# Optimization experiments

Hardware: AMD Instinct MI355X
Metric: run time of the kernel (lower is better)

## Reference

```python
import jax, jax.numpy as jnp
import numpy as np

B, N, E_PER = 512, 256, 8192          # graphs, nodes per graph, edges per graph
FIN, H, K, FOUT = 128, 32, 16, 10     # in_channels, hidden, num clusters, out_channels
EPS = 1e-15


def setup_inputs() -> dict:
    key = jax.random.key(0)
    ks = jax.random.split(key, 12)
    x = jax.random.normal(ks[0], (B * N, FIN), jnp.float32)
    # intra-graph random edges, then offset into the global node index space
    src = jax.random.randint(ks[1], (B, E_PER), 0, N)
    dst = jax.random.randint(ks[2], (B, E_PER), 0, N)
    offs = (jnp.arange(B) * N)[:, None]
    edge_index = jnp.stack([(src + offs).reshape(-1), (dst + offs).reshape(-1)]).astype(jnp.int64)
    batch = jnp.repeat(jnp.arange(B), N).astype(jnp.int64)

    def lin(k, fin, fout):
        return (jax.random.normal(k, (fin, fout), jnp.float32) / np.sqrt(fin)).astype(jnp.float32)

    params = {
        'W_lin1': lin(ks[3], FIN, H), 'b_lin1': jnp.zeros((H,), jnp.float32),
        'W_rel1': lin(ks[4], H, H), 'b_rel1': jnp.zeros((H,), jnp.float32),
        'W_root1': lin(ks[5], H, H),
        'W_pool': lin(ks[6], H, K), 'b_pool': jnp.zeros((K,), jnp.float32),
        'W_rel2': lin(ks[7], H, H), 'b_rel2': jnp.zeros((H,), jnp.float32),
        'W_root2': lin(ks[8], H, H),
        'W_lin2': lin(ks[9], H, H), 'b_lin2': jnp.zeros((H,), jnp.float32),
        'W_lin3': lin(ks[10], H, FOUT), 'b_lin3': jnp.zeros((FOUT,), jnp.float32),
    }
    return {'x': x, 'edge_index': edge_index, 'batch': batch, **params}


def _densify(x, edge_index, batch):
    """to_dense_adj + to_dense_batch: [total,F] -> [B,N,F], [B,N,N], [B,N]."""
    n_total = x.shape[0]
    counts = jax.ops.segment_sum(jnp.ones((n_total,), jnp.int32), batch, num_segments=B)
    offsets = jnp.concatenate([jnp.zeros((1,), jnp.int32), jnp.cumsum(counts)[:-1]])
    pos = jnp.arange(n_total) - offsets[batch]            # position of node inside its graph
    eb = batch[edge_index[0]]                             # graph id of each edge
    adj = jnp.zeros((B, N, N), jnp.float32).at[eb, pos[edge_index[0]], pos[edge_index[1]]].add(1.0)
    xd = jnp.zeros((B, N, x.shape[1]), jnp.float32).at[batch, pos].set(x)
    mask = jnp.zeros((B, N), jnp.float32).at[batch, pos].set(1.0)
    return xd, adj, mask


def _dense_graph_conv(x, adj, W_rel, b_rel, W_root):
    # PyG DenseGraphConv(aggr='add'): lin_rel(adj @ x) + lin_root(x)
    return jnp.einsum('bnm,bmh,hk->bnk', adj, x, W_rel) + b_rel + x @ W_root


def _dense_mincut_pool(x, adj, s, mask):
    s = jax.nn.softmax(s, axis=-1)
    x = x * mask[..., None]
    s = s * mask[..., None]
    out = jnp.einsum('bnk,bnh->bkh', s, x)                        # s^T x
    out_adj = jnp.einsum('bnk,bnm,bmj->bkj', s, adj, s)           # s^T A s
    mincut_num = jnp.einsum('bkk->b', out_adj)
    d_flat = adj.sum(-1)                                          # degree
    mincut_den = jnp.einsum('bnk,bn,bnk->b', s, d_flat, s)        # trace(s^T D s)
    mincut_loss = jnp.mean(-(mincut_num / mincut_den))
    ss = jnp.einsum('bnk,bnj->bkj', s, s)
    ss_norm = jnp.linalg.norm(ss, axis=(-1, -2), keepdims=True)
    i_s = jnp.eye(K, dtype=jnp.float32)
    ortho_loss = jnp.mean(jnp.linalg.norm(ss / ss_norm - i_s / jnp.sqrt(jnp.float32(K)), axis=(-1, -2)))
    # zero diagonal, symmetric degree normalization
    diag_mask = 1.0 - i_s
    out_adj = out_adj * diag_mask
    d = jnp.sqrt(out_adj.sum(-1))[:, None, :] + EPS               # [B,1,K]
    out_adj = out_adj / d / jnp.swapaxes(d, 1, 2)
    return out, out_adj, mincut_loss, ortho_loss


def reference(x, edge_index, batch, W_lin1, b_lin1, W_rel1, b_rel1, W_root1,
              W_pool, b_pool, W_rel2, b_rel2, W_root2, W_lin2, b_lin2, W_lin3, b_lin3):
    xd, adj, mask = _densify(x, edge_index, batch)
    h = xd @ W_lin1 + b_lin1                                      # lin1
    h = _dense_graph_conv(h, adj, W_rel1, b_rel1, W_root1)        # conv1
    s2 = h @ W_pool + b_pool                                      # pool2
    h, adj_p, mincut_loss2, ortho_loss2 = _dense_mincut_pool(h, adj, s2, mask)
    h = _dense_graph_conv(h, adj_p, W_rel2, b_rel2, W_root2)      # conv2
    h = h.sum(axis=1)                                             # readout sum over clusters
    h = jax.nn.relu(h @ W_lin2 + b_lin2)
    h = h @ W_lin3 + b_lin3
    return jax.nn.log_softmax(h, axis=-1), mincut_loss2, ortho_loss2
```

## Files before the change

### kernel.cpp

```cpp
#include <hip/hip_runtime.h>

#define NB 512
#define NN 256
#define EPG 8192
#define FINC 128

typedef float f32x4 __attribute__((ext_vector_type(4)));
typedef short s16x8 __attribute__((ext_vector_type(8)));

__device__ __forceinline__ float bf2f(unsigned short u) {
  union { unsigned int i; float f; } x; x.i = ((unsigned int)u) << 16; return x.f;
}
__device__ __forceinline__ unsigned short f2bf(float f) {
  union { float f; unsigned int i; } x; x.f = f;
  unsigned int r = x.i + 0x7fffu + ((x.i >> 16) & 1u);
  return (unsigned short)(r >> 16);
}
__device__ __forceinline__ short ftrunc_bf(float f) {
  union { float f; unsigned int i; } x; x.f = f;
  return (short)(x.i >> 16);
}

struct Params {
  const void* x; const void* ei;
  const void *wl1, *bl1, *wr1, *br1, *wro1, *wp, *bp;
  const void *wr2, *br2, *wro2, *wl2, *bl2, *wl3, *bl3;
  float* out; float* ws;
};

__device__ __forceinline__ bool detect_bf16(const void* p) {
  const unsigned short* pw = (const unsigned short*)p;
  int sane = 0;
  for (int i = 0; i < 64; ++i) {
    unsigned e = (pw[i] >> 7) & 0xFFu;
    sane += (e > 96u && e < 132u) ? 1 : 0;
  }
  return sane >= 56;
}
__device__ __forceinline__ bool detect_i64(const void* p) {
  const int* pi = (const int*)p + EPG;
  int ok = 0;
  for (int i = 0; i < 32; ++i) ok += (pi[i] >= 256 && pi[i] < 512) ? 1 : 0;
  return ok < 24;
}
__device__ __forceinline__ float ldf(const void* p, int i, bool bf) {
  return bf ? bf2f(((const unsigned short*)p)[i]) : ((const float*)p)[i];
}

#define SMEM_TOTAL 81920

__global__ __launch_bounds__(1024, 8) void mincut_main(Params P) {
  extern __shared__ char smem[];
  const int t = threadIdx.x;
  const int b = blockIdx.x;

  const bool BF  = detect_bf16(P.wr1);
  const bool I64 = detect_i64(P.ei);

  float* pbufH  = (float*)(smem + 0);
  float* pbufL  = (float*)(smem + 2048);
  float* oadjH  = (float*)(smem + 4096);
  float* oadjL  = (float*)(smem + 5120);
  float* ssA    = (float*)(smem + 6144);
  float* pbuf   = (float*)(smem + 7168);
  float* oadjb  = (float*)(smem + 9216);
  unsigned short* h0T  = (unsigned short*)(smem + 33792);
  unsigned short* yTl  = (unsigned short*)(smem + 33792);
  unsigned short* h1Th = (unsigned short*)(smem + 33792);
  unsigned short* w1t  = (unsigned short*)(smem + 50688);
  unsigned short* zT   = (unsigned short*)(smem + 50688);
  unsigned short* sTh  = (unsigned short*)(smem + 50688);
  unsigned short* sTl  = (unsigned short*)(smem + 59136);
  unsigned short* wrelTh = (unsigned short*)(smem + 67584);
  unsigned short* wrelTl = (unsigned short*)(smem + 70144);
  unsigned short* wrootT = (unsigned short*)(smem + 72704);
  float* blin1f = (float*)(smem + 75264);
  unsigned short* yTh = (unsigned short*)(smem + 67584);
  unsigned short* taT = (unsigned short*)(smem + 67584);
  unsigned short* wpoolTh = (unsigned short*)(smem + 76032);
  unsigned short* wpoolTl = (unsigned short*)(smem + 77184);
  unsigned short* m1Th    = (unsigned short*)(smem + 78336);
  unsigned short* m1Tl    = (unsigned short*)(smem + 79488);
  float*          scrE    = (float*)(smem + 79488);
  unsigned short* m2Th    = (unsigned short*)(smem + 80640);
  float*          bMf     = (float*)(smem + 81792);
  unsigned short* brel1h  = (unsigned short*)(smem + 81856);

  const int wv = t >> 6, lane = t & 63;
  const int lm = lane & 15, quad = lane >> 4;
  const int mbase = wv * 16;

  {
    uint4 z = {0u, 0u, 0u, 0u};
    for (int i = t; i < 2112; i += 1024) ((uint4*)smem)[i] = z;
  }
  for (int e = t; e < 4096; e += 1024) {
    int k = e >> 5, c = e & 31;
    w1t[c * 136 + k] = f2bf(ldf(P.wl1, e, BF));
  }
  {
    int k = t >> 5, c = t & 31;
    float wr = ldf(P.wr1, t, BF);
    unsigned short hi = f2bf(wr);
    wrelTh[c * 40 + k] = hi;
    wrelTl[c * 40 + k] = f2bf(wr - bf2f(hi));
    wrootT[c * 40 + k] = f2bf(ldf(P.wro1, t, BF));
  }
  if (t < 512) {
    int m = t >> 4, c = t & 15;
    float w = ldf(P.wp, t, BF);
    unsigned short hi = f2bf(w);
    wpoolTh[c * 36 + m] = hi;
    wpoolTl[c * 36 + m] = f2bf(w - bf2f(hi));
  }
  if (t < 32) { blin1f[t] = ldf(P.bl1, t, BF); brel1h[t] = f2bf(ldf(P.br1, t, BF)); }
  __syncthreads();

  if (I64) {
    const uint4* s4 = (const uint4*)((const long long*)P.ei + (size_t)b * EPG) + t * 4;
    const uint4* d4 = (const uint4*)((const long long*)P.ei + (size_t)NB * EPG + (size_t)b * EPG) + t * 4;
    #pragma unroll
    for (int i = 0; i < 4; ++i) {
      uint4 a = s4[i], c = d4[i];
      unsigned n0 = (a.x & 255u) * 264u + (c.x & 255u);
      unsigned n1 = (a.z & 255u) * 264u + (c.z & 255u);
      atomicAdd((unsigned int*)(smem + ((n0 >> 3) << 2)), 1u << ((n0 & 7u) * 4u));
      atomicAdd((unsigned int*)(smem + ((n1 >> 3) << 2)), 1u << ((n1 & 7u) * 4u));
    }
  } else {
    const uint4* s4 = (const uint4*)((const int*)P.ei + (size_t)b * EPG) + t * 2;
    const uint4* d4 = (const uint4*)((const int*)P.ei + (size_t)NB * EPG + (size_t)b * EPG) + t * 2;
    #pragma unroll
    for (int i = 0; i < 2; ++i) {
      uint4 a = s4[i], c = d4[i];
      unsigned n0 = (a.x & 255u) * 264u + (c.x & 255u);
      unsigned n1 = (a.y & 255u) * 264u + (c.y & 255u);
      unsigned n2 = (a.z & 255u) * 264u + (c.z & 255u);
      unsigned n3 = (a.w & 255u) * 264u + (c.w & 255u);
      atomicAdd((unsigned int*)(smem + ((n0 >> 3) << 2)), 1u << ((n0 & 7u) * 4u));
      atomicAdd((unsigned int*)(smem + ((n1 >> 3) << 2)), 1u << ((n1 & 7u) * 4u));
      atomicAdd((unsigned int*)(smem + ((n2 >> 3) << 2)), 1u << ((n2 & 7u) * 4u));
      atomicAdd((unsigned int*)(smem + ((n3 >> 3) << 2)), 1u << ((n3 & 7u) * 4u));
    }
  }

  {
    f32x4 acc[2] = {{0.f,0.f,0.f,0.f},{0.f,0.f,0.f,0.f}};
    const size_t node = (size_t)(b * 256 + mbase + lm);
    #pragma unroll
    for (int ks = 0; ks < 4; ++ks) {
      const int k0 = ks * 32 + quad * 8;
      s16x8 a;
      if (BF) {
        a = *(const s16x8*)((const unsigned short*)P.x + node * 128 + k0);
      } else {
        const float* xp = (const float*)P.x + node * 128 + k0;
        f32x4 v0 = *(const f32x4*)xp;
        f32x4 v1 = *(const f32x4*)(xp + 4);
        #pragma unroll
        for (int j = 0; j < 4; ++j) { a[j] = (short)f2bf(v0[j]); a[4 + j] = (short)f2bf(v1[j]); }
      }
      #pragma unroll
      for (int ct = 0; ct < 2; ++ct) {
        s16x8 bh = *(const s16x8*)(w1t + (ct * 16 + lm) * 136 + k0);
        acc[ct] = __builtin_amdgcn_mfma_f32_16x16x32_bf16(a, bh, acc[ct], 0, 0, 0);
      }
    }
    #pragma unroll
    for (int ct = 0; ct < 2; ++ct) {
      const int c = ct * 16 + lm;
      float bias = blin1f[c];
      #pragma unroll
      for (int r = 0; r < 4; ++r)
        h0T[c * 264 + mbase + quad * 4 + r] = f2bf(acc[ct][r] + bias);
    }
  }

  if (wv == 2 || wv == 3) {
    const int mb = (wv - 2) * 16;
    s16x8 Ah, Al;
    #pragma unroll
    for (int j = 0; j < 8; ++j) {
      int k = quad * 8 + j;
      Ah[j] = (short)wrelTh[k * 40 + mb + lm];
      Al[j] = (short)wrelTl[k * 40 + mb + lm];
    }
    s16x8 Bh, Bl;
    ((uint2*)&Bh)[0] = *(const uint2*)(wpoolTh + lm * 36 + quad * 8);
    ((uint2*)&Bh)[1] = *(const uint2*)(wpoolTh + lm * 36 + quad * 8 + 4);
    ((uint2*)&Bl)[0] = *(const uint2*)(wpoolTl + lm * 36 + quad * 8);
    ((uint2*)&Bl)[1] = *(const uint2*)(wpoolTl + lm * 36 + quad * 8 + 4);
    f32x4 acc = {0.f, 0.f, 0.f, 0.f};
    acc = __builtin_amdgcn_mfma_f32_16x16x32_bf16(Ah, Bh, acc, 0, 0, 0);
    acc = __builtin_amdgcn_mfma_f32_16x16x32_bf16(Al, Bh, acc, 0, 0, 0);
    acc = __builtin_amdgcn_mfma_f32_16x16x32_bf16(Ah, Bl, acc, 0, 0, 0);
    #pragma unroll
    for (int r = 0; r < 4; ++r) {
      int m = mb + quad * 4 + r;
      unsigned short hi = f2bf(acc[r]);
      m1Th[lm * 36 + m] = hi;
      m1Tl[lm * 36 + m] = f2bf(acc[r] - bf2f(hi));
    }
  }
  if (wv == 4 || wv == 5) {
    const int mb = (wv - 4) * 16;
    s16x8 Ah;
    #pragma unroll
    for (int j = 0; j < 8; ++j) Ah[j] = (short)wrootT[(quad * 8 + j) * 40 + mb + lm];
    s16x8 Bh, Bl;
    ((uint2*)&Bh)[0] = *(const uint2*)(wpoolTh + lm * 36 + quad * 8);
    ((uint2*)&Bh)[1] = *(const uint2*)(wpoolTh + lm * 36 + quad * 8 + 4);
    ((uint2*)&Bl)[0] = *(const uint2*)(wpoolTl + lm * 36 + quad * 8);
    ((uint2*)&Bl)[1] = *(const uint2*)(wpoolTl + lm * 36 + quad * 8 + 4);
    f32x4 acc = {0.f, 0.f, 0.f, 0.f};
    acc = __builtin_amdgcn_mfma_f32_16x16x32_bf16(Ah, Bh, acc, 0, 0, 0);
    acc = __builtin_amdgcn_mfma_f32_16x16x32_bf16(Ah, Bl, acc, 0, 0, 0);
    #pragma unroll
    for (int r = 0; r < 4; ++r) m2Th[lm * 36 + (mb + quad * 4 + r)] = f2bf(acc[r]);
  }
  if (wv == 6 && lane < 16) {
    float acc = ldf(P.bp, lane, BF);
    #pragma unroll 8
    for (int m = 0; m < 32; ++m)
      acc += bf2f(brel1h[m]) * (bf2f(wpoolTh[lane * 36 + m]) + bf2f(wpoolTl[lane * 36 + m]));
    bMf[lane] = acc;
  }
  __syncthreads();

  f32x4 racc[2] = {{0.f,0.f,0.f,0.f},{0.f,0.f,0.f,0.f}};
  f32x4 yacc = {0.f,0.f,0.f,0.f}, macc = {0.f,0.f,0.f,0.f};
  {
    s16x8 Ah;
    #pragma unroll
    for (int j = 0; j < 8; ++j) Ah[j] = (short)h0T[(quad * 8 + j) * 264 + mbase + lm];
    f32x4 zacc[2] = {{0.f,0.f,0.f,0.f},{0.f,0.f,0.f,0.f}};
    #pragma unroll
    for (int ct = 0; ct < 2; ++ct) {
      const int c = ct * 16 + lm;
      s16x8 brh = *(const s16x8*)(wrelTh + c * 40 + quad * 8);
      s16x8 brl = *(const s16x8*)(wrelTl + c * 40 + quad * 8);
      s16x8 bro = *(const s16x8*)(wrootT + c * 40 + quad * 8);
      zacc[ct] = __builtin_amdgcn_mfma_f32_16x16x32_bf16(Ah, brh, zacc[ct], 0, 0, 0);
      zacc[ct] = __builtin_amdgcn_mfma_f32_16x16x32_bf16(Ah, brl, zacc[ct], 0, 0, 0);
      racc[ct] = __builtin_amdgcn_mfma_f32_16x16x32_bf16(Ah, bro, racc[ct], 0, 0, 0);
    }
    s16x8 Bm1h, Bm1l, Bm2;
    ((uint2*)&Bm1h)[0] = *(const uint2*)(m1Th + lm * 36 + quad * 8);
    ((uint2*)&Bm1h)[1] = *(const uint2*)(m1Th + lm * 36 + quad * 8 + 4);
    ((uint2*)&Bm1l)[0] = *(const uint2*)(m1Tl + lm * 36 + quad * 8);
    ((uint2*)&Bm1l)[1] = *(const uint2*)(m1Tl + lm * 36 + quad * 8 + 4);
    ((uint2*)&Bm2)[0]  = *(const uint2*)(m2Th + lm * 36 + quad * 8);
    ((uint2*)&Bm2)[1]  = *(const uint2*)(m2Th + lm * 36 + quad * 8 + 4);
    yacc = __builtin_amdgcn_mfma_f32_16x16x32_bf16(Ah, Bm1h, yacc, 0, 0, 0);
    yacc = __builtin_amdgcn_mfma_f32_16x16x32_bf16(Ah, Bm1l, yacc, 0, 0, 0);
    macc = __builtin_amdgcn_mfma_f32_16x16x32_bf16(Ah, Bm2, macc, 0, 0, 0);
    #pragma unroll
    for (int ct = 0; ct < 2; ++ct)
      #pragma unroll
      for (int r = 0; r < 4; ++r)
        zT[(ct * 16 + lm) * 264 + mbase + quad * 4 + r] = f2bf(zacc[ct][r]);
  }
  __syncthreads();

  #pragma unroll
  for (int r = 0; r < 4; ++r) {
    int node = mbase + quad * 4 + r;
    unsigned short hi = f2bf(yacc[r]);
    yTh[lm * 264 + node] = hi;
    yTl[lm * 264 + node] = f2bf(yacc[r] - bf2f(hi));
  }
  __syncthreads();

  f32x4 h1v[2], sval;
  {
    f32x4 h1acc[2] = { racc[0], racc[1] };
    f32x4 lacc = macc;
    unsigned dsum = 0;
    const char* arow = smem + (mbase + lm) * 132;
    #pragma unroll
    for (int ks = 0; ks < 8; ++ks) {
      unsigned d = *(const unsigned int*)(arow + ks * 16 + quad * 4);
      unsigned v = (d & 0x0F0F0F0Fu) + ((d >> 4) & 0x0F0F0F0Fu);
      dsum += (v * 0x01010101u) >> 24;
      s16x8 af;
      #pragma unroll
      for (int j = 0; j < 8; ++j) af[j] = ftrunc_bf((float)((d >> (4 * j)) & 15u));
      const int v0 = ks * 32 + quad * 8;
      #pragma unroll
      for (int ct = 0; ct < 2; ++ct) {
        s16x8 bz = *(const s16x8*)(zT + (ct * 16 + lm) * 264 + v0);
        h1acc[ct] = __builtin_amdgcn_mfma_f32_16x16x32_bf16(af, bz, h1acc[ct], 0, 0, 0);
      }
      s16x8 byh = *(const s16x8*)(yTh + lm * 264 + v0);
      s16x8 byl = *(const s16x8*)(yTl + lm * 264 + v0);
      lacc = __builtin_amdgcn_mfma_f32_16x16x32_bf16(af, byh, lacc, 0, 0, 0);
      lacc = __builtin_amdgcn_mfma_f32_16x16x32_bf16(af, byl, lacc, 0, 0, 0);
    }
    dsum += __shfl_xor(dsum, 16, 64);
    dsum += __shfl_xor(dsum, 32, 64);
    float degf = (float)dsum;
    #pragma unroll
    for (int ct = 0; ct < 2; ++ct) {
      float bias = bf2f(brel1h[ct * 16 + lm]);
      #pragma unroll
      for (int r = 0; r < 4; ++r) h1v[ct][r] = h1acc[ct][r] + bias;
    }
    f32x4 lg;
    float bm = bMf[lm];
    #pragma unroll
    for (int r = 0; r < 4; ++r) lg[r] = lacc[r] + bm;
    f32x4 mx = lg;
    #pragma unroll
    for (int m = 1; m <= 8; m <<= 1)
      #pragma unroll
      for (int r = 0; r < 4; ++r) mx[r] = fmaxf(mx[r], __shfl_xor(mx[r], m, 64));
    #pragma unroll
    for (int r = 0; r < 4; ++r) lg[r] = __expf(lg[r] - mx[r]);
    f32x4 sm = lg;
    #pragma unroll
    for (int m = 1; m <= 8; m <<= 1)
      #pragma unroll
      for (int r = 0; r < 4; ++r) sm[r] += __shfl_xor(sm[r], m, 64);
    f32x4 sq;
    #pragma unroll
    for (int r = 0; r < 4; ++r) { sval[r] = lg[r] / sm[r]; sq[r] = sval[r] * sval[r]; }
    #pragma unroll
    for (int m = 1; m <= 8; m <<= 1)
      #pragma unroll
      for (int r = 0; r < 4; ++r) sq[r] += __shfl_xor(sq[r], m, 64);
    {
      int l = lane & 15, src = (l >> 2) << 4;
      float q0 = __shfl(sq[0], src, 64), q1 = __shfl(sq[1], src, 64);
      float q2 = __shfl(sq[2], src, 64), q3 = __shfl(sq[3], src, 64);
      float ssel = (l & 2) ? ((l & 1) ? q3 : q2) : ((l & 1) ? q1 : q0);
      float vden = (lane < 16) ? degf * ssel : 0.f;
      #pragma unroll
      for (int o = 32; o > 0; o >>= 1) vden += __shfl_xor(vden, o, 64);
      if (lane == 0) scrE[wv] = vden;
    }
  }
  __syncthreads();

  #pragma unroll
  for (int ct = 0; ct < 2; ++ct)
    #pragma unroll
    for (int r = 0; r < 4; ++r)
      h1Th[(ct * 16 + lm) * 264 + mbase + quad * 4 + r] = f2bf(h1v[ct][r]);
  #pragma unroll
  for (int r = 0; r < 4; ++r) {
    int node = mbase + quad * 4 + r;
    unsigned short hi = f2bf(sval[r]);
    sTh[lm * 264 + node] = hi;
    sTl[lm * 264 + node] = f2bf(sval[r] - bf2f(hi));
  }
  __syncthreads();

  {
    f32x4 tacc = {0.f, 0.f, 0.f, 0.f};
    const char* arow = smem + (mbase + lm) * 132;
    #pragma unroll
    for (int ks = 0; ks < 8; ++ks) {
      unsigned d = *(const unsigned int*)(arow + ks * 16 + quad * 4);
      s16x8 af;
      #pragma unroll
      for (int j = 0; j < 8; ++j) af[j] = ftrunc_bf((float)((d >> (4 * j)) & 15u));
      const int v0 = ks * 32 + quad * 8;
      s16x8 bh = *(const s16x8*)(sTh + lm * 264 + v0);
      s16x8 bl = *(const s16x8*)(sTl + lm * 264 + v0);
      tacc = __builtin_amdgcn_mfma_f32_16x16x32_bf16(af, bh, tacc, 0, 0, 0);
      tacc = __builtin_amdgcn_mfma_f32_16x16x32_bf16(af, bl, tacc, 0, 0, 0);
    }
    #pragma unroll
    for (int r = 0; r < 4; ++r) taT[lm * 264 + mbase + quad * 4 + r] = f2bf(tacc[r]);
  }
  __syncthreads();

  if (wv < 7) {
    const unsigned short *Ap, *Bp; float* dst; int W, ct = 0;
    switch (wv) {
      case 0: Ap = sTh; Bp = h1Th; dst = pbufH; W = 32; ct = 0; break;
      case 1: Ap = sTh; Bp = h1Th; dst = pbufH; W = 32; ct = 1; break;
      case 2: Ap = sTl; Bp = h1Th; dst = pbufL; W = 32; ct = 0; break;
      case 3: Ap = sTl; Bp = h1Th; dst = pbufL; W = 32; ct = 1; break;
      case 4: Ap = sTh; Bp = taT;  dst = oadjH; W = 16; break;
      case 5: Ap = sTl; Bp = taT;  dst = oadjL; W = 16; break;
      default: Ap = sTh; Bp = sTh; dst = ssA;   W = 16; break;
    }
    const int cidx = ct * 16 + lm;
    const unsigned short* Bb = Bp + cidx * 264;
    f32x4 acc = {0.f, 0.f, 0.f, 0.f};
    #pragma unroll
    for (int ch = 0; ch < 8; ++ch) {
      s16x8 a = *(const s16x8*)(Ap + lm * 264 + ch * 32 + quad * 8);
      s16x8 bb = *(const s16x8*)(Bb + ch * 32 + quad * 8);
      acc = __builtin_amdgcn_mfma_f32_16x16x32_bf16(a, bb, acc, 0, 0, 0);
    }
    #pragma unroll
    for (int r = 0; r < 4; ++r) dst[(quad * 4 + r) * W + cidx] = acc[r];
  }
  __syncthreads();

  if (wv != 0) return;

  for (int i = lane; i < 512; i += 64) pbuf[i] = pbufH[i] + pbufL[i];
  for (int i = lane; i < 256; i += 64) oadjb[i] = oadjH[i] + oadjL[i];

  {
    float vden = (lane < 16) ? scrE[lane] : 0.f;
    float vnum = (lane < 16) ? oadjb[lane * 17] : 0.f;
    float vtr  = (lane < 16) ? ssA[lane * 17] : 0.f;
    float vfro = 0.f;
    #pragma unroll
    for (int i = 0; i < 4; ++i) { float v = ssA[lane + i * 64]; vfro += v * v; }
    #pragma unroll
    for (int o = 32; o > 0; o >>= 1) {
      vden += __shfl_xor(vden, o, 64);
      vnum += __shfl_xor(vnum, o, 64);
      vfro += __shfl_xor(vfro, o, 64);
      vtr  += __shfl_xor(vtr, o, 64);
    }
    if (lane == 0) {
      float ssn = sqrtf(vfro);
      float orth2 = 2.f - vtr / (2.f * ssn);
      atomicAdd(P.ws, -(vnum / vden) * (1.f / NB));
      atomicAdd(P.ws + 1, sqrtf(fmaxf(orth2, 0.f)) * (1.f / NB));
    }
  }

  float uv;
  {
    const int l16 = lane & 15;
    float rs = 0.f;
    #pragma unroll
    for (int j = 0; j < 16; ++j) if (j != l16) rs += oadjb[l16 * 16 + j];
    float ddv = sqrtf(rs) + 1e-15f;
    float s = 0.f;
    #pragma unroll
    for (int k = 0; k < 16; ++k) {
      float ddk = __shfl(ddv, k, 64);
      if (k != l16) s += oadjb[k * 16 + l16] / ddk;
    }
    uv = s / ddv;
  }

  float Qv = 0.f, Pv = 0.f;
  {
    const int m = lane & 31;
    #pragma unroll
    for (int j = 0; j < 16; ++j) {
      float uj = __shfl(uv, j, 64);
      float pj = pbuf[j * 32 + m];
      Qv += uj * pj;
      Pv += pj;
    }
  }

  float rbv;
  {
    const int c = lane & 31;
    float acc = 16.f * ldf(P.br2, c, BF);
    #pragma unroll 8
    for (int m = 0; m < 32; ++m) {
      float qm = __shfl(Qv, m, 64);
      float pm = __shfl(Pv, m, 64);
      acc += qm * ldf(P.wr2, m * 32 + c, BF) + pm * ldf(P.wro2, m * 32 + c, BF);
    }
    rbv = acc;
  }
  float yv;
  {
    const int c = lane & 31;
    float acc = ldf(P.bl2, c, BF);
    #pragma unroll 8
    for (int m = 0; m < 32; ++m)
      acc += __shfl(rbv, m, 64) * ldf(P.wl2, m * 32 + c, BF);
    yv = fmaxf(acc, 0.f);
  }
  {
    const int c10 = (lane < 10) ? lane : 0;
    float lg = ldf(P.bl3, c10, BF);
    #pragma unroll 8
    for (int m = 0; m < 32; ++m)
      lg += __shfl(yv, m, 64) * ldf(P.wl3, m * 10 + c10, BF);
    float lgm = (lane < 10) ? lg : -3.4e38f;
    #pragma unroll
    for (int o = 1; o <= 8; o <<= 1) lgm = fmaxf(lgm, __shfl_xor(lgm, o, 64));
    float ex = (lane < 10) ? __expf(lg - lgm) : 0.f;
    #pragma unroll
    for (int o = 1; o <= 8; o <<= 1) ex += __shfl_xor(ex, o, 64);
    float lse = lgm + __logf(ex);
    if (lane < 10) {
      float val = lg - lse;
      if (BF) ((unsigned short*)P.out)[b * 10 + lane] = f2bf(val);
      else    P.out[b * 10 + lane] = val;
    }
  }

  if (lane == 0) {
    __threadfence();
    unsigned cnt = atomicAdd((unsigned int*)(P.ws + 2), 1u);
    if (cnt == NB - 1) {
      float l0 = atomicAdd(P.ws, 0.f);
      float l1 = atomicAdd(P.ws + 1, 0.f);
      if (BF) {
        ((unsigned short*)P.out)[5120] = f2bf(l0);
        ((unsigned short*)P.out)[5121] = f2bf(l1);
      } else {
        P.out[5120] = l0;
        P.out[5121] = l1;
      }
    }
  }
}

extern "C" void kernel_launch(void* const* d_in, const int* in_sizes, int n_in,
                              void* d_out, int out_size, void* d_ws, size_t ws_size,
                              hipStream_t stream) {
  (void)in_sizes; (void)n_in; (void)out_size; (void)ws_size;
  Params P;
  P.x    = d_in[0];
  P.ei   = d_in[1];
  P.wl1  = d_in[3];
  P.bl1  = d_in[4];
  P.wr1  = d_in[5];
  P.br1  = d_in[6];
  P.wro1 = d_in[7];
  P.wp   = d_in[8];
  P.bp   = d_in[9];
  P.wr2  = d_in[10];
  P.br2  = d_in[11];
  P.wro2 = d_in[12];
  P.wl2  = d_in[13];
  P.bl2  = d_in[14];
  P.wl3  = d_in[15];
  P.bl3  = d_in[16];
  P.out  = (float*)d_out;
  P.ws   = (float*)d_ws;

  hipMemsetAsync(d_ws, 0, 3 * sizeof(float), stream);
  hipFuncSetAttribute(reinterpret_cast<const void*>(mincut_main),
                      hipFuncAttributeMaxDynamicSharedMemorySize, SMEM_TOTAL);
  hipLaunchKernelGGL(mincut_main, dim3(NB), dim3(1024), SMEM_TOTAL, stream, P);
}
```

Baseline: 175.8 us.

## Stage tail weights in LDS, cache adjacency words, parallelize tail reductions

All 1024 threads now stage the second-stage weights and biases (rel2, root2, lin2, lin3 and their biases) into shared memory before the final barrier. The serial single-wave tail then reads them from LDS instead of issuing dependent global loads. The packed adjacency words are kept in registers between the two adjacency matmuls, so the second pass does not reload them from LDS. The loss reductions and row sums are spread over all waves and combined through a small scratch buffer, and divisions become reciprocal multiplies. The cost is more registers and a reorganized shared-memory layout, which may affect occupancy.

```diff
diff --git a/kernel.cpp b/kernel.cpp
--- a/kernel.cpp
+++ b/kernel.cpp
@@ -57,13 +57,21 @@
   const bool BF  = detect_bf16(P.wr1);
   const bool I64 = detect_i64(P.ei);
 
-  float* pbufH  = (float*)(smem + 0);
-  float* pbufL  = (float*)(smem + 2048);
-  float* oadjH  = (float*)(smem + 4096);
-  float* oadjL  = (float*)(smem + 5120);
-  float* ssA    = (float*)(smem + 6144);
-  float* pbuf   = (float*)(smem + 7168);
-  float* oadjb  = (float*)(smem + 9216);
+  float* pbuf   = (float*)(smem + 0);
+  float* oadjb  = (float*)(smem + 2048);
+  float* scr    = (float*)(smem + 8704);
+  float* rel2f  = (float*)(smem + 9216);
+  float* root2f = (float*)(smem + 13312);
+  float* lin2f  = (float*)(smem + 17408);
+  float* lin3f  = (float*)(smem + 21504);
+  float* brel2f = (float*)(smem + 22784);
+  float* blin2f = (float*)(smem + 22912);
+  float* blin3f = (float*)(smem + 23040);
+  float* pbufH  = (float*)(smem + 24576);
+  float* pbufL  = (float*)(smem + 26624);
+  float* oadjH  = (float*)(smem + 28672);
+  float* oadjL  = (float*)(smem + 29696);
+  float* ssA    = (float*)(smem + 30720);
   unsigned short* h0T  = (unsigned short*)(smem + 33792);
   unsigned short* yTl  = (unsigned short*)(smem + 33792);
   unsigned short* h1Th = (unsigned short*)(smem + 33792);
@@ -272,6 +280,7 @@
   __syncthreads();
 
   f32x4 h1v[2], sval;
+  unsigned adjw[8];
   {
     f32x4 h1acc[2] = { racc[0], racc[1] };
     f32x4 lacc = macc;
@@ -280,6 +289,7 @@
     #pragma unroll
     for (int ks = 0; ks < 8; ++ks) {
       unsigned d = *(const unsigned int*)(arow + ks * 16 + quad * 4);
+      adjw[ks] = d;
       unsigned v = (d & 0x0F0F0F0Fu) + ((d >> 4) & 0x0F0F0F0Fu);
       dsum += (v * 0x01010101u) >> 24;
       s16x8 af;
@@ -357,10 +367,9 @@
 
   {
     f32x4 tacc = {0.f, 0.f, 0.f, 0.f};
-    const char* arow = smem + (mbase + lm) * 132;
     #pragma unroll
     for (int ks = 0; ks < 8; ++ks) {
-      unsigned d = *(const unsigned int*)(arow + ks * 16 + quad * 4);
+      unsigned d = adjw[ks];
       s16x8 af;
       #pragma unroll
       for (int j = 0; j < 8; ++j) af[j] = ftrunc_bf((float)((d >> (4 * j)) & 15u));
@@ -374,6 +383,14 @@
     for (int r = 0; r < 4; ++r) taT[lm * 264 + mbase + quad * 4 + r] = f2bf(tacc[r]);
   }
   __syncthreads();
+
+  rel2f[t] = ldf(P.wr2, t, BF);
+  root2f[t] = ldf(P.wro2, t, BF);
+  lin2f[t] = ldf(P.wl2, t, BF);
+  if (t < 320) lin3f[t] = ldf(P.wl3, t, BF);
+  if (t < 32) brel2f[t] = ldf(P.br2, t, BF);
+  if (t < 32) blin2f[t] = ldf(P.bl2, t, BF);
+  if (t < 10) blin3f[t] = ldf(P.bl3, t, BF);
 
   if (wv < 7) {
     const unsigned short *Ap, *Bp; float* dst; int W, ct = 0;
@@ -400,49 +417,54 @@
   }
   __syncthreads();
 
-  if (wv != 0) return;
-
-  for (int i = lane; i < 512; i += 64) pbuf[i] = pbufH[i] + pbufL[i];
-  for (int i = lane; i < 256; i += 64) oadjb[i] = oadjH[i] + oadjL[i];
-
-  {
-    float vden = (lane < 16) ? scrE[lane] : 0.f;
-    float vnum = (lane < 16) ? oadjb[lane * 17] : 0.f;
-    float vtr  = (lane < 16) ? ssA[lane * 17] : 0.f;
-    float vfro = 0.f;
-    #pragma unroll
-    for (int i = 0; i < 4; ++i) { float v = ssA[lane + i * 64]; vfro += v * v; }
+  float rs = 0.f;
+  if (t < 512) {
+    pbuf[t] = pbufH[t] + pbufL[t];
+  } else if (t < 768) {
+    int i = t - 512; oadjb[i] = oadjH[i] + oadjL[i];
+  }
+  {
+    float vnum = (t < 16) ? (oadjH[t * 17] + oadjL[t * 17]) : 0.f;
+    float vfro = (t < 256) ? ssA[t] * ssA[t] : 0.f;
+    float vtr  = (t < 16) ? ssA[t * 17] : 0.f;
     #pragma unroll
     for (int o = 32; o > 0; o >>= 1) {
-      vden += __shfl_xor(vden, o, 64);
       vnum += __shfl_xor(vnum, o, 64);
       vfro += __shfl_xor(vfro, o, 64);
       vtr  += __shfl_xor(vtr, o, 64);
     }
-    if (lane == 0) {
-      float ssn = sqrtf(vfro);
-      float orth2 = 2.f - vtr / (2.f * ssn);
-      atomicAdd(P.ws, -(vnum / vden) * (1.f / NB));
-      atomicAdd(P.ws + 1, sqrtf(fmaxf(orth2, 0.f)) * (1.f / NB));
-    }
-  }
-
+    if (lane == 0) { scr[16 + wv] = vnum; scr[32 + wv] = vfro; scr[48 + wv] = vtr; }
+  }
+  if (wv == 0 && lane < 16) {
+    #pragma unroll
+    for (int j = 0; j < 16; ++j)
+      if (j != lane) rs += oadjH[lane * 16 + j] + oadjL[lane * 16 + j];
+  }
+  __syncthreads();
+
+  if (wv != 0) return;
+
+  if (lane == 0) {
+    float den = 0.f, num = 0.f, fro = 0.f, tr = 0.f;
+    #pragma unroll
+    for (int i = 0; i < 16; ++i) { den += scrE[i]; num += scr[16 + i]; fro += scr[32 + i]; tr += scr[48 + i]; }
+    float ssn = sqrtf(fro);
+    float orth2 = 2.f - tr / (2.f * ssn);
+    atomicAdd(P.ws, -(num / den) * (1.f / NB));
+    atomicAdd(P.ws + 1, sqrtf(fmaxf(orth2, 0.f)) * (1.f / NB));
+  }
+  float iddv = (lane < 16) ? 1.f / (sqrtf(rs) + 1e-15f) : 0.f;
   float uv;
   {
     const int l16 = lane & 15;
-    float rs = 0.f;
-    #pragma unroll
-    for (int j = 0; j < 16; ++j) if (j != l16) rs += oadjb[l16 * 16 + j];
-    float ddv = sqrtf(rs) + 1e-15f;
     float s = 0.f;
     #pragma unroll
     for (int k = 0; k < 16; ++k) {
-      float ddk = __shfl(ddv, k, 64);
-      if (k != l16) s += oadjb[k * 16 + l16] / ddk;
-    }
-    uv = s / ddv;
-  }
-
+      float iddk = __shfl(iddv, k, 64);
+      if (k != l16) s += oadjb[k * 16 + l16] * iddk;
+    }
+    uv = s * __shfl(iddv, l16, 64);
+  }
   float Qv = 0.f, Pv = 0.f;
   {
     const int m = lane & 31;
@@ -454,34 +476,31 @@
       Pv += pj;
     }
   }
-
   float rbv;
   {
     const int c = lane & 31;
-    float acc = 16.f * ldf(P.br2, c, BF);
+    float acc = 16.f * brel2f[c];
     #pragma unroll 8
     for (int m = 0; m < 32; ++m) {
-      float qm = __shfl(Qv, m, 64);
-      float pm = __shfl(Pv, m, 64);
-      acc += qm * ldf(P.wr2, m * 32 + c, BF) + pm * ldf(P.wro2, m * 32 + c, BF);
+      acc += __shfl(Qv, m, 64) * rel2f[m * 32 + c] + __shfl(Pv, m, 64) * root2f[m * 32 + c];
     }
     rbv = acc;
   }
   float yv;
   {
     const int c = lane & 31;
-    float acc = ldf(P.bl2, c, BF);
+    float acc = blin2f[c];
     #pragma unroll 8
     for (int m = 0; m < 32; ++m)
-      acc += __shfl(rbv, m, 64) * ldf(P.wl2, m * 32 + c, BF);
+      acc += __shfl(rbv, m, 64) * lin2f[m * 32 + c];
     yv = fmaxf(acc, 0.f);
   }
   {
     const int c10 = (lane < 10) ? lane : 0;
-    float lg = ldf(P.bl3, c10, BF);
+    float lg = blin3f[c10];
     #pragma unroll 8
     for (int m = 0; m < 32; ++m)
-      lg += __shfl(yv, m, 64) * ldf(P.wl3, m * 10 + c10, BF);
+      lg += __shfl(yv, m, 64) * lin3f[m * 10 + c10];
     float lgm = (lane < 10) ? lg : -3.4e38f;
     #pragma unroll
     for (int o = 1; o <= 8; o <<= 1) lgm = fmaxf(lgm, __shfl_xor(lgm, o, 64));
@@ -495,7 +514,6 @@
       else    P.out[b * 10 + lane] = val;
     }
   }
-
   if (lane == 0) {
     __threadfence();
     unsigned cnt = atomicAdd((unsigned int*)(P.ws + 2), 1u);
```

Result: slower. 198.4 us (+12.9%).
